# Optimization experiments

Hardware: AMD Instinct MI355X
Metric: run time of the kernel (lower is better)

The kernel has to match this reference:

```python
import jax, jax.numpy as jnp
import numpy as np

FCM_ITERS = 3
FCM_M = 2.0
EPS = 1e-8


def batched_index_select(x, idx):
    # x: [B, C, M, 1], idx: [B, N, K] -> [B, C, N, K]
    xt = x[..., 0]  # [B, C, M]
    return jnp.take_along_axis(xt[:, :, None, :], idx[:, None, :, :], axis=3)


def fcm_centroids(x, num_clusters):
    # Fuzzy c-means soft clustering (HyperedgeConstruction).
    # x: [B, C, N, 1] -> centroids [B, C, K], weights [B, N, 1, K]
    xt = jnp.transpose(x[..., 0], (0, 2, 1))  # [B, N, C]
    B, N, C = xt.shape
    init_idx = jnp.linspace(0, N - 1, num_clusters).astype(jnp.int32)
    cent = xt[:, init_idx, :]  # [B, K, C] deterministic init
    expo = -1.0 / (FCM_M - 1.0)

    def memberships(cent):
        xn = jnp.sum(xt * xt, axis=-1)            # [B, N]
        cn = jnp.sum(cent * cent, axis=-1)        # [B, K]
        d2 = xn[:, :, None] + cn[:, None, :] - 2.0 * jnp.einsum('bnc,bkc->bnk', xt, cent)
        d2 = jnp.maximum(d2, EPS)
        inv = d2 ** expo
        return inv / jnp.sum(inv, axis=-1, keepdims=True)  # [B, N, K]

    for _ in range(FCM_ITERS):
        u = memberships(cent)
        um = u ** FCM_M
        cent = jnp.einsum('bnk,bnc->bkc', um, xt) / (jnp.sum(um, axis=1)[..., None] + EPS)
    u = memberships(cent)
    centroids = jnp.transpose(cent, (0, 2, 1))  # [B, C, K]
    return centroids, u[:, :, None, :]          # weights [B, N, 1, K]


def setup_inputs() -> dict:
    key = jax.random.key(0)
    k1, k2, k3, k4 = jax.random.split(key, 4)
    B, C, N, K = 4, 64, 8192, 16
    OC = 64
    return {
        "x": jax.random.normal(k1, (B, C, N, 1), jnp.float32),
        "edge_index": jax.random.randint(k2, (2, B, N, K), 0, N),
        "W": jax.random.normal(k3, (OC, 3 * C), jnp.float32) / np.sqrt(3 * C).astype(np.float32),
        "b": jax.random.normal(k4, (OC,), jnp.float32) * 0.01,
        "num_clusters": 50,
        "top_clusters": 5,
    }


def reference(x, edge_index, W, b, num_clusters, top_clusters):
    B, C, N, _ = x.shape
    # max-relative neighbor feature
    x_i = batched_index_select(x, edge_index[1])          # [B, C, N, K]
    x_j = batched_index_select(x, edge_index[0])          # [B, C, N, K]
    x_j = jnp.max(x_j - x_i, axis=-1, keepdims=True)      # [B, C, N, 1]
    # soft-cluster (hyperedge) feature
    centroids, weights = fcm_centroids(x, num_clusters)   # [B,C,K], [B,N,1,K]
    weights = weights[:, :, 0, :]                         # squeeze(-2) -> [B, N, K]
    _, nn_idx_centroid = jax.lax.top_k(weights, top_clusters)  # [B, N, top]
    x_j_cluster = batched_index_select(centroids[..., None], nn_idx_centroid)  # [B, C, N, top]
    # x gathered at center_idx == x broadcast over top dim
    x_j_cluster = jnp.max(x_j_cluster - x, axis=-1, keepdims=True)  # [B, C, N, 1]
    # interleaved concat: [B, C, 3, N, 1] -> [B, 3C, N, 1]
    feat = jnp.stack([x, x_j, x_j_cluster], axis=2).reshape(B, 3 * C, N, 1)
    # BasicConv: 1x1 conv + ReLU
    out = jnp.einsum('oc,bcni->boni', W, feat) + b[None, :, None, None]
    return jax.nn.relu(out)
```

## Files before the change

kernel.cpp:

```cpp
#include <hip/hip_runtime.h>


constexpr int B  = 4;
constexpr int C  = 64;
constexpr int N  = 8192;
constexpr int KE = 16;
constexpr int OC = 64;
constexpr int NC = 50;
constexpr int TC = 5;
constexpr int C3 = 192;
constexpr int NSL = 128;
constexpr float FEPS = 1e-8f;

__global__ __launch_bounds__(256) void k_transpose(const float* __restrict__ x,
                                                   float* __restrict__ xt,
                                                   float* __restrict__ xn) {
  __shared__ float tile[64][65];
  int b  = blockIdx.x >> 7;
  int n0 = (blockIdx.x & 127) << 6;
  int tid = threadIdx.x;
  int nl = tid & 63, cq = tid >> 6;
#pragma unroll
  for (int r = 0; r < 16; ++r) {
    int cc = r * 4 + cq;
    tile[cc][nl] = x[((size_t)b * C + cc) * N + n0 + nl];
  }
  __syncthreads();
  int cl = tid & 63, nq = tid >> 6;
#pragma unroll
  for (int r = 0; r < 16; ++r) {
    int nr = r * 4 + nq;
    xt[((size_t)b * N + n0 + nr) * C + cl] = tile[cl][nr];
  }
  if (tid < 64) {
    float s = 0.f;
#pragma unroll
    for (int cc = 0; cc < 64; ++cc) { float v = tile[cc][tid]; s = fmaf(v, v, s); }
    xn[(size_t)b * N + n0 + tid] = s;
  }
}

__global__ __launch_bounds__(256) void k_init(const float* __restrict__ xt,
                                              float* __restrict__ cent,
                                              float* __restrict__ cn) {
  int i = blockIdx.x * 256 + threadIdx.x;
  int lane = threadIdx.x & 63;
  int ccol = i & 63;
  int row  = i >> 6;
  int k = row % NC, b = row / NC;
  int src = (k * (N - 1)) / (NC - 1);
  float v = xt[((size_t)b * N + src) * C + ccol];
  cent[i] = v;
  float sq = v * v;
#pragma unroll
  for (int off = 32; off; off >>= 1) sq += __shfl_down(sq, off, 64);
  if (lane == 0) cn[row] = sq;
}

__global__ __launch_bounds__(512) void k_fcm(const float* __restrict__ xt,
                                             const float* __restrict__ xn,
                                             const float* __restrict__ cent,
                                             const float* __restrict__ cn,
                                             float* __restrict__ pc,
                                             float* __restrict__ pu) {
  __shared__ float s_xt[64][68];
  __shared__ float s_u[NC][64];
  __shared__ float s_ps[8][64];
  int gid = blockIdx.x;
  int xcd = gid & 7;
  int b = xcd >> 1;
  int chunk = ((gid >> 3) << 1) + (xcd & 1);
  int n0 = chunk << 6;
  int w = __builtin_amdgcn_readfirstlane((int)threadIdx.x >> 6);
  int lane = threadIdx.x & 63;
  int n = n0 + lane;
  int base = (w < 2) ? 7 * w : 14 + 6 * (w - 2);
  int cnt  = (w < 2) ? 7 : 6;
  const float* xr = xt + ((size_t)b * N + n) * C;
  const float* cb = cent + b * NC * C;
  float dot[7];
#pragma unroll
  for (int j = 0; j < 7; ++j) dot[j] = 0.f;
  for (int c4 = 0; c4 < C; c4 += 4) {
    float4 xv = *(const float4*)(xr + c4);
    if (w == 0) *(float4*)(&s_xt[lane][c4]) = xv;
#pragma unroll
    for (int j = 0; j < 7; ++j) {
      int kk = base + j; kk = (kk < NC) ? kk : 0;
      float4 cv = *(const float4*)(cb + kk * C + c4);
      dot[j] = fmaf(xv.x, cv.x, dot[j]);
      dot[j] = fmaf(xv.y, cv.y, dot[j]);
      dot[j] = fmaf(xv.z, cv.z, dot[j]);
      dot[j] = fmaf(xv.w, cv.w, dot[j]);
    }
  }
  float xnv = xn[(size_t)b * N + n];
  const float* cnb = cn + b * NC;
  float inv[7];
  float psum = 0.f;
#pragma unroll
  for (int j = 0; j < 7; ++j) {
    int kk = base + j; kk = (kk < NC) ? kk : 0;
    float d2 = fmaf(-2.f, dot[j], xnv + cnb[kk]);
    d2 = fmaxf(d2, FEPS);
    float iv = 1.f / d2;
    inv[j] = iv;
    psum += (j < cnt) ? iv : 0.f;
  }
  s_ps[w][lane] = psum;
  __syncthreads();
  float ssum = 0.f;
#pragma unroll
  for (int ww = 0; ww < 8; ++ww) ssum += s_ps[ww][lane];
  float s2i = 1.f / (ssum * ssum);
#pragma unroll
  for (int j = 0; j < 7; ++j)
    if (j < cnt) s_u[base + j][lane] = inv[j] * inv[j] * s2i;
  __syncthreads();
  int c = lane;
  float acc[7], ua[7];
#pragma unroll
  for (int j = 0; j < 7; ++j) { acc[j] = 0.f; ua[j] = 0.f; }
  for (int nn = 0; nn < 64; ++nn) {
    float xv = s_xt[nn][c];
#pragma unroll
    for (int j = 0; j < 7; ++j) {
      int kk = base + j; kk = (kk < NC) ? kk : 0;
      float u = s_u[kk][nn];
      acc[j] = fmaf(u, xv, acc[j]);
      ua[j] += u;
    }
  }
  float* pcb = pc + (((size_t)chunk * (B * NC) + b * NC + base)) * C + c;
#pragma unroll
  for (int j = 0; j < 7; ++j)
    if (j < cnt) pcb[(size_t)j * C] = acc[j];
  if (lane == 0) {
#pragma unroll
    for (int j = 0; j < 7; ++j)
      if (j < cnt) pu[(size_t)chunk * (B * NC) + b * NC + base + j] = ua[j];
  }
}

__global__ __launch_bounds__(256) void k_m3(const float* __restrict__ pc,
                                            const float* __restrict__ pu,
                                            float* __restrict__ cent,
                                            float* __restrict__ cn) {
  int i = blockIdx.x * 256 + threadIdx.x;
  int lane = threadIdx.x & 63;
  int row = i >> 6;
  float tot = 0.f;
#pragma unroll 16
  for (int s = 0; s < NSL; ++s) tot += pc[(size_t)s * (B * NC * C) + i];
  float us = 0.f;
#pragma unroll 16
  for (int s = 0; s < NSL; ++s) us += pu[(size_t)s * (B * NC) + row];
  float v = tot / (us + FEPS);
  cent[i] = v;
  float sq = v * v;
#pragma unroll
  for (int off = 32; off; off >>= 1) sq += __shfl_down(sq, off, 64);
  if (lane == 0) cn[row] = sq;
}

__global__ __launch_bounds__(512) void k_top5(const float* __restrict__ xt,
                                              const float* __restrict__ xn,
                                              const float* __restrict__ cent,
                                              const float* __restrict__ cn,
                                              int* __restrict__ t5) {
  int gid = blockIdx.x;
  int xcd = gid & 7;
  int b = xcd >> 1;
  int chunk = ((gid >> 3) << 1) + (xcd & 1);
  int n0 = chunk << 6;
  int w = __builtin_amdgcn_readfirstlane((int)threadIdx.x >> 6);
  int lane = threadIdx.x & 63;
  int n = n0 + lane;
  int base = (w < 2) ? 7 * w : 14 + 6 * (w - 2);
  int cnt  = (w < 2) ? 7 : 6;
  const float* xr = xt + ((size_t)b * N + n) * C;
  const float* cb = cent + b * NC * C;
  float dot[7];
#pragma unroll
  for (int j = 0; j < 7; ++j) dot[j] = 0.f;
  for (int c4 = 0; c4 < C; c4 += 4) {
    float4 xv = *(const float4*)(xr + c4);
#pragma unroll
    for (int j = 0; j < 7; ++j) {
      int kk = base + j; kk = (kk < NC) ? kk : 0;
      float4 cv = *(const float4*)(cb + kk * C + c4);
      dot[j] = fmaf(xv.x, cv.x, dot[j]);
      dot[j] = fmaf(xv.y, cv.y, dot[j]);
      dot[j] = fmaf(xv.z, cv.z, dot[j]);
      dot[j] = fmaf(xv.w, cv.w, dot[j]);
    }
  }
  float xnv = xn[(size_t)b * N + n];
  const float* cnb = cn + b * NC;
  __shared__ float s_inv[NC][65];
#pragma unroll
  for (int j = 0; j < 7; ++j) {
    int kk = base + j; kk = (kk < NC) ? kk : 0;
    float d2 = fmaxf(fmaf(-2.f, dot[j], xnv + cnb[kk]), FEPS);
    float iv = 1.f / d2;
    if (j < cnt) s_inv[base + j][lane] = iv;
  }
  __syncthreads();
  if (w == 0) {
    float v[NC];
#pragma unroll
    for (int k = 0; k < NC; ++k) v[k] = s_inv[k][lane];
    unsigned long long taken = 0ull;
    int* tp = t5 + ((size_t)b * N + n) * TC;
#pragma unroll
    for (int t = 0; t < TC; ++t) {
      float best = -1.f;
      int bi = 0;
#pragma unroll
      for (int k = 0; k < NC; ++k) {
        bool ok = (((taken >> k) & 1ull) == 0ull) && (v[k] > best);
        best = ok ? v[k] : best;
        bi   = ok ? k : bi;
      }
      taken |= (1ull << bi);
      tp[t] = bi;
    }
  }
}

__global__ __launch_bounds__(512, 4) void k_out(const float* __restrict__ xt,
                                                const float* __restrict__ cent,
                                                const float* __restrict__ W,
                                                const int* __restrict__ t5,
                                                const int* __restrict__ eidx,
                                                const float* __restrict__ bias,
                                                float* __restrict__ out) {
  __shared__ float s_feat[C3][65];
  int tid = threadIdx.x;
  int gid = blockIdx.x;
  int xcd = gid & 7;
  int b = xcd >> 1;
  int chunk = ((gid >> 3) << 1) + (xcd & 1);
  int wv = __builtin_amdgcn_readfirstlane(tid >> 6);
  int lane = tid & 63;
  int n0 = chunk * 64;
  int nw0 = n0 + wv * 8;
  const float* xtb = xt + ((size_t)b * N) * C;
  const float* cb  = cent + b * NC * C;
  const int* e0b = eidx + ((size_t)b * N) * KE;
  const int* e1b = eidx + ((size_t)(B + b) * N) * KE;
  int c = lane;
  int fr = wv * 8;
#pragma unroll
  for (int j = 0; j < 8; ++j) {
    int n = nw0 + j;
    const int* p0 = e0b + (size_t)n * KE;
    const int* p1 = e1b + (size_t)n * KE;
    const int* tp = t5 + ((size_t)b * N + n) * TC;
    float x0 = xtb[(size_t)n * C + c];
    float g0[KE], g1[KE];
#pragma unroll
    for (int k = 0; k < KE; ++k) {
      g0[k] = xtb[(size_t)p0[k] * C + c];
      g1[k] = xtb[(size_t)p1[k] * C + c];
    }
    float cv[TC];
#pragma unroll
    for (int t = 0; t < TC; ++t) cv[t] = cb[(size_t)tp[t] * C + c];
    float m1 = g0[0] - g1[0];
#pragma unroll
    for (int k = 1; k < KE; ++k) m1 = fmaxf(m1, g0[k] - g1[k]);
    float cm = cv[0];
#pragma unroll
    for (int t = 1; t < TC; ++t) cm = fmaxf(cm, cv[t]);
    s_feat[3 * c + 0][fr + j] = x0;
    s_feat[3 * c + 1][fr + j] = m1;
    s_feat[3 * c + 2][fr + j] = cm - x0;
  }
  __syncthreads();
  int o0 = wv * 8;
  float acc[8];
#pragma unroll
  for (int oj = 0; oj < 8; ++oj) acc[oj] = bias[o0 + oj];
#pragma unroll 4
  for (int f = 0; f < C3; ++f) {
    float v = s_feat[f][lane];
#pragma unroll
    for (int oj = 0; oj < 8; ++oj)
      acc[oj] = fmaf(W[(size_t)(o0 + oj) * C3 + f], v, acc[oj]);
  }
  float* ob = out + ((size_t)b * OC + o0) * N + n0 + lane;
#pragma unroll
  for (int oj = 0; oj < 8; ++oj)
    ob[(size_t)oj * N] = fmaxf(acc[oj], 0.f);
}

extern "C" void kernel_launch(void* const* d_in, const int* in_sizes, int n_in,
                              void* d_out, int out_size, void* d_ws, size_t ws_size,
                              hipStream_t stream) {
  const float* x    = (const float*)d_in[0];
  const int*   eidx = (const int*)d_in[1];
  const float* W    = (const float*)d_in[2];
  const float* bias = (const float*)d_in[3];

  float* ws   = (float*)d_ws;
  float* xt   = ws;
  float* xn   = xt + (size_t)B * N * C;
  float* cent = xn + (size_t)B * N;
  float* cn   = cent + B * NC * C;
  float* pc   = cn + 256;
  float* pu   = pc + (size_t)NSL * B * NC * C;
  int*   t5   = (int*)(pu + (size_t)NSL * B * NC);
  float* out  = (float*)d_out;

  k_transpose<<<dim3(B * (N / 64)), dim3(256), 0, stream>>>(x, xt, xn);
  k_init<<<dim3((B * NC * C) / 256), dim3(256), 0, stream>>>(xt, cent, cn);
  for (int it = 0; it < 3; ++it) {
    k_fcm<<<dim3(512), dim3(512), 0, stream>>>(xt, xn, cent, cn, pc, pu);
    k_m3<<<dim3((B * NC * C) / 256), dim3(256), 0, stream>>>(pc, pu, cent, cn);
  }
  k_top5<<<dim3(512), dim3(512), 0, stream>>>(xt, xn, cent, cn, t5);
  k_out<<<dim3(512), dim3(512), 0, stream>>>(xt, cent, W, t5, eidx, bias, out);
}
```

Baseline: 232.9 us.

## Fuse top-5 cluster selection into output kernel; compute membership sums via shuffles

```diff
diff --git a/kernel.cpp b/kernel.cpp
--- a/kernel.cpp
+++ b/kernel.cpp
@@ -114,13 +114,21 @@
   for (int ww = 0; ww < 8; ++ww) ssum += s_ps[ww][lane];
   float s2i = 1.f / (ssum * ssum);
 #pragma unroll
-  for (int j = 0; j < 7; ++j)
-    if (j < cnt) s_u[base + j][lane] = inv[j] * inv[j] * s2i;
+  for (int j = 0; j < 7; ++j) {
+    float uval = inv[j] * inv[j] * s2i;
+    if (j < cnt) s_u[base + j][lane] = uval;
+    float r = (j < cnt) ? uval : 0.f;
+#pragma unroll
+    for (int off = 32; off; off >>= 1) r += __shfl_down(r, off, 64);
+    if (lane == 0 && j < cnt)
+      pu[(size_t)chunk * (B * NC) + b * NC + base + j] = r;
+  }
   __syncthreads();
   int c = lane;
-  float acc[7], ua[7];
-#pragma unroll
-  for (int j = 0; j < 7; ++j) { acc[j] = 0.f; ua[j] = 0.f; }
+  float acc[7];
+#pragma unroll
+  for (int j = 0; j < 7; ++j) acc[j] = 0.f;
+#pragma unroll 8
   for (int nn = 0; nn < 64; ++nn) {
     float xv = s_xt[nn][c];
 #pragma unroll
@@ -128,18 +136,12 @@
       int kk = base + j; kk = (kk < NC) ? kk : 0;
       float u = s_u[kk][nn];
       acc[j] = fmaf(u, xv, acc[j]);
-      ua[j] += u;
     }
   }
   float* pcb = pc + (((size_t)chunk * (B * NC) + b * NC + base)) * C + c;
 #pragma unroll
   for (int j = 0; j < 7; ++j)
     if (j < cnt) pcb[(size_t)j * C] = acc[j];
-  if (lane == 0) {
-#pragma unroll
-    for (int j = 0; j < 7; ++j)
-      if (j < cnt) pu[(size_t)chunk * (B * NC) + b * NC + base + j] = ua[j];
-  }
 }
 
 __global__ __launch_bounds__(256) void k_m3(const float* __restrict__ pc,
@@ -163,79 +165,17 @@
   if (lane == 0) cn[row] = sq;
 }
 
-__global__ __launch_bounds__(512) void k_top5(const float* __restrict__ xt,
-                                              const float* __restrict__ xn,
-                                              const float* __restrict__ cent,
-                                              const float* __restrict__ cn,
-                                              int* __restrict__ t5) {
-  int gid = blockIdx.x;
-  int xcd = gid & 7;
-  int b = xcd >> 1;
-  int chunk = ((gid >> 3) << 1) + (xcd & 1);
-  int n0 = chunk << 6;
-  int w = __builtin_amdgcn_readfirstlane((int)threadIdx.x >> 6);
-  int lane = threadIdx.x & 63;
-  int n = n0 + lane;
-  int base = (w < 2) ? 7 * w : 14 + 6 * (w - 2);
-  int cnt  = (w < 2) ? 7 : 6;
-  const float* xr = xt + ((size_t)b * N + n) * C;
-  const float* cb = cent + b * NC * C;
-  float dot[7];
-#pragma unroll
-  for (int j = 0; j < 7; ++j) dot[j] = 0.f;
-  for (int c4 = 0; c4 < C; c4 += 4) {
-    float4 xv = *(const float4*)(xr + c4);
-#pragma unroll
-    for (int j = 0; j < 7; ++j) {
-      int kk = base + j; kk = (kk < NC) ? kk : 0;
-      float4 cv = *(const float4*)(cb + kk * C + c4);
-      dot[j] = fmaf(xv.x, cv.x, dot[j]);
-      dot[j] = fmaf(xv.y, cv.y, dot[j]);
-      dot[j] = fmaf(xv.z, cv.z, dot[j]);
-      dot[j] = fmaf(xv.w, cv.w, dot[j]);
-    }
-  }
-  float xnv = xn[(size_t)b * N + n];
-  const float* cnb = cn + b * NC;
-  __shared__ float s_inv[NC][65];
-#pragma unroll
-  for (int j = 0; j < 7; ++j) {
-    int kk = base + j; kk = (kk < NC) ? kk : 0;
-    float d2 = fmaxf(fmaf(-2.f, dot[j], xnv + cnb[kk]), FEPS);
-    float iv = 1.f / d2;
-    if (j < cnt) s_inv[base + j][lane] = iv;
-  }
-  __syncthreads();
-  if (w == 0) {
-    float v[NC];
-#pragma unroll
-    for (int k = 0; k < NC; ++k) v[k] = s_inv[k][lane];
-    unsigned long long taken = 0ull;
-    int* tp = t5 + ((size_t)b * N + n) * TC;
-#pragma unroll
-    for (int t = 0; t < TC; ++t) {
-      float best = -1.f;
-      int bi = 0;
-#pragma unroll
-      for (int k = 0; k < NC; ++k) {
-        bool ok = (((taken >> k) & 1ull) == 0ull) && (v[k] > best);
-        best = ok ? v[k] : best;
-        bi   = ok ? k : bi;
-      }
-      taken |= (1ull << bi);
-      tp[t] = bi;
-    }
-  }
-}
-
-__global__ __launch_bounds__(512, 4) void k_out(const float* __restrict__ xt,
-                                                const float* __restrict__ cent,
-                                                const float* __restrict__ W,
-                                                const int* __restrict__ t5,
-                                                const int* __restrict__ eidx,
-                                                const float* __restrict__ bias,
-                                                float* __restrict__ out) {
+__global__ __launch_bounds__(512, 4) void k_out5(const float* __restrict__ xt,
+                                                 const float* __restrict__ xn,
+                                                 const float* __restrict__ cent,
+                                                 const float* __restrict__ cn,
+                                                 const float* __restrict__ W,
+                                                 const int* __restrict__ eidx,
+                                                 const float* __restrict__ bias,
+                                                 float* __restrict__ out) {
   __shared__ float s_feat[C3][65];
+  __shared__ int s_t5[64][TC];
+  float (*s_inv)[65] = s_feat;
   int tid = threadIdx.x;
   int gid = blockIdx.x;
   int xcd = gid & 7;
@@ -244,9 +184,60 @@
   int wv = __builtin_amdgcn_readfirstlane(tid >> 6);
   int lane = tid & 63;
   int n0 = chunk * 64;
-  int nw0 = n0 + wv * 8;
   const float* xtb = xt + ((size_t)b * N) * C;
   const float* cb  = cent + b * NC * C;
+  {
+    int n = n0 + lane;
+    int base = (wv < 2) ? 7 * wv : 14 + 6 * (wv - 2);
+    int cnt  = (wv < 2) ? 7 : 6;
+    const float* xr = xtb + (size_t)n * C;
+    float dot[7];
+#pragma unroll
+    for (int j = 0; j < 7; ++j) dot[j] = 0.f;
+    for (int c4 = 0; c4 < C; c4 += 4) {
+      float4 xv = *(const float4*)(xr + c4);
+#pragma unroll
+      for (int j = 0; j < 7; ++j) {
+        int kk = base + j; kk = (kk < NC) ? kk : 0;
+        float4 cv = *(const float4*)(cb + kk * C + c4);
+        dot[j] = fmaf(xv.x, cv.x, dot[j]);
+        dot[j] = fmaf(xv.y, cv.y, dot[j]);
+        dot[j] = fmaf(xv.z, cv.z, dot[j]);
+        dot[j] = fmaf(xv.w, cv.w, dot[j]);
+      }
+    }
+    float xnv = xn[(size_t)b * N + n];
+    const float* cnb = cn + b * NC;
+#pragma unroll
+    for (int j = 0; j < 7; ++j) {
+      int kk = base + j; kk = (kk < NC) ? kk : 0;
+      float d2 = fmaxf(fmaf(-2.f, dot[j], xnv + cnb[kk]), FEPS);
+      float iv = 1.f / d2;
+      if (j < cnt) s_inv[base + j][lane] = iv;
+    }
+  }
+  __syncthreads();
+  if (wv == 0) {
+    float v[NC];
+#pragma unroll
+    for (int k = 0; k < NC; ++k) v[k] = s_inv[k][lane];
+    unsigned long long taken = 0ull;
+#pragma unroll
+    for (int t = 0; t < TC; ++t) {
+      float best = -1.f;
+      int bi = 0;
+#pragma unroll
+      for (int k = 0; k < NC; ++k) {
+        bool ok = (((taken >> k) & 1ull) == 0ull) && (v[k] > best);
+        best = ok ? v[k] : best;
+        bi   = ok ? k : bi;
+      }
+      taken |= (1ull << bi);
+      s_t5[lane][t] = bi;
+    }
+  }
+  __syncthreads();
+  int nw0 = n0 + wv * 8;
   const int* e0b = eidx + ((size_t)b * N) * KE;
   const int* e1b = eidx + ((size_t)(B + b) * N) * KE;
   int c = lane;
@@ -256,7 +247,8 @@
     int n = nw0 + j;
     const int* p0 = e0b + (size_t)n * KE;
     const int* p1 = e1b + (size_t)n * KE;
-    const int* tp = t5 + ((size_t)b * N + n) * TC;
+    int t0 = s_t5[fr + j][0], t1 = s_t5[fr + j][1], t2 = s_t5[fr + j][2];
+    int t3 = s_t5[fr + j][3], t4 = s_t5[fr + j][4];
     float x0 = xtb[(size_t)n * C + c];
     float g0[KE], g1[KE];
 #pragma unroll
@@ -264,15 +256,13 @@
       g0[k] = xtb[(size_t)p0[k] * C + c];
       g1[k] = xtb[(size_t)p1[k] * C + c];
     }
-    float cv[TC];
-#pragma unroll
-    for (int t = 0; t < TC; ++t) cv[t] = cb[(size_t)tp[t] * C + c];
+    float cv0 = cb[(size_t)t0 * C + c], cv1 = cb[(size_t)t1 * C + c];
+    float cv2 = cb[(size_t)t2 * C + c], cv3 = cb[(size_t)t3 * C + c];
+    float cv4 = cb[(size_t)t4 * C + c];
     float m1 = g0[0] - g1[0];
 #pragma unroll
     for (int k = 1; k < KE; ++k) m1 = fmaxf(m1, g0[k] - g1[k]);
-    float cm = cv[0];
-#pragma unroll
-    for (int t = 1; t < TC; ++t) cm = fmaxf(cm, cv[t]);
+    float cm = fmaxf(fmaxf(fmaxf(fmaxf(cv0, cv1), cv2), cv3), cv4);
     s_feat[3 * c + 0][fr + j] = x0;
     s_feat[3 * c + 1][fr + j] = m1;
     s_feat[3 * c + 2][fr + j] = cm - x0;
@@ -310,7 +300,6 @@
   float* cn   = cent + B * NC * C;
   float* pc   = cn + 256;
   float* pu   = pc + (size_t)NSL * B * NC * C;
-  int*   t5   = (int*)(pu + (size_t)NSL * B * NC);
   float* out  = (float*)d_out;
 
   k_transpose<<<dim3(B * (N / 64)), dim3(256), 0, stream>>>(x, xt, xn);
@@ -319,6 +308,5 @@
     k_fcm<<<dim3(512), dim3(512), 0, stream>>>(xt, xn, cent, cn, pc, pu);
     k_m3<<<dim3((B * NC * C) / 256), dim3(256), 0, stream>>>(pc, pu, cent, cn);
   }
-  k_top5<<<dim3(512), dim3(512), 0, stream>>>(xt, xn, cent, cn, t5);
-  k_out<<<dim3(512), dim3(512), 0, stream>>>(xt, cent, W, t5, eidx, bias, out);
-}
+  k_out5<<<dim3(512), dim3(512), 0, stream>>>(xt, xn, cent, cn, W, eidx, bias, out);
+}
```

Measured after the change: 227.2 us. -2.4%, faster.
